# Performance work log

Hardware: AMD Instinct MI355X
Metric: run time of the kernel (lower is better)

The kernel has to match this reference:

```python
import jax, jax.numpy as jnp
import numpy as np

EPS = 1.1920929e-07  # torch clamp_probs eps for float32
TEMP = 0.3           # sampler temperature T


def conv1d(x, w, b, pad):
    # x: [B, Cin, L], w: [Cout, Cin, K] -> [B, Cout, L']
    y = jax.lax.conv_general_dilated(x, w, window_strides=(1,), padding=[(pad, pad)],
                                     dimension_numbers=('NCH', 'OIH', 'NCH'))
    return y + b[None, :, None]


def setup_inputs() -> dict:
    key = jax.random.key(0)
    ks = jax.random.split(key, 20)
    B, L, V, E, F, H, K = 512, 512, 100000, 100, 100, 100, 10
    p = lambda i, shape: jax.random.normal(ks[i], shape, jnp.float32) * 0.02
    return {
        'x': jax.random.randint(ks[0], (B, L), 0, V, dtype=jnp.int32),
        'u': jax.random.uniform(ks[1], (B, K, L), dtype=jnp.float32),
        'emb': p(2, (V, E)),
        'conv1_w': p(3, (F, E, 3)), 'conv1_b': p(4, (F,)),
        'gi_w': p(5, (H, F)), 'gi_b': p(6, (H,)),
        'conv2_w': p(7, (H, F, 3)), 'conv2_b': p(8, (H,)),
        'li_w': p(9, (H, H, 3)), 'li_b': p(10, (H,)),
        'conv3_w': p(11, (F, 2 * H, 1)), 'conv3_b': p(12, (F,)),
        'conv4_w': p(13, (1, F, 1)), 'conv4_b': p(14, (1,)),
        'fc1_w': p(15, (H, E)), 'fc1_b': p(16, (H,)),
        'head_w': p(17, (1, H)), 'head_b': p(18, (1,)),
    }


def _ti_logits(e, conv1_w, conv1_b, gi_w, gi_b, conv2_w, conv2_b,
               li_w, li_b, conv3_w, conv3_b, conv4_w, conv4_b):
    relu = jax.nn.relu
    xt = jnp.swapaxes(e, 1, 2)                       # [B, E, L]
    h = relu(conv1d(xt, conv1_w, conv1_b, 1))        # [B, F, L]
    g = relu(h.mean(axis=-1) @ gi_w.T + gi_b)        # [B, H] (AdaptiveAvgPool1d(1))
    loc = relu(conv1d(relu(conv1d(h, conv2_w, conv2_b, 1)), li_w, li_b, 1))  # [B, H, L]
    gexp = jnp.broadcast_to(g[:, :, None], loc.shape)
    z = jnp.concatenate([gexp, loc], axis=1)         # [B, 2H, L]
    z = relu(conv1d(z, conv3_w, conv3_b, 0))
    return conv1d(z, conv4_w, conv4_b, 0)            # [B, 1, L]


def reference(x, u, emb, conv1_w, conv1_b, gi_w, gi_b, conv2_w, conv2_b,
              li_w, li_b, conv3_w, conv3_b, conv4_w, conv4_b,
              fc1_w, fc1_b, head_w, head_b):
    e = emb[x]                                       # [B, L, E] embedding gather
    logits = _ti_logits(e, conv1_w, conv1_b, gi_w, gi_b, conv2_w, conv2_b,
                        li_w, li_b, conv3_w, conv3_b, conv4_w, conv4_b)
    # Gumbel top-k continuous sampling (training path)
    uc = jnp.clip(u, EPS, 1.0 - EPS)
    gumbel = -jnp.log(-jnp.log(uc))                  # [B, K, L]
    noisy = (gumbel + logits) / TEMP                 # logits [B,1,L] broadcasts over K
    csamples = jax.nn.softmax(noisy, axis=-1).max(axis=1)  # [B, L]
    # distil predictor: masked mean pooling + MLP + sigmoid head
    pooled = (e * csamples[:, :, None]).mean(axis=1)  # [B, E]
    h = jax.nn.relu(pooled @ fc1_w.T + fc1_b)
    out = jax.nn.sigmoid(h @ head_w.T + head_b)       # [B, 1]
    return out, csamples
```

## Files before the change

kernel.cpp:

```cpp
#include <hip/hip_runtime.h>
#include <math.h>

#define DEV __device__ __forceinline__

typedef __attribute__((ext_vector_type(8))) short short8;
typedef __attribute__((ext_vector_type(4))) short short4v;
typedef __attribute__((ext_vector_type(4))) float f32x4;
typedef __attribute__((ext_vector_type(2))) unsigned uint2v;

#define SSTR 136
#define ROWB (16 * SSTR * 2)

DEV short f2bf(float f) {
    unsigned u = __builtin_bit_cast(unsigned, f);
    unsigned r = (u + 0x7fffu + ((u >> 16) & 1u)) >> 16;
    return (short)r;
}

#if __has_builtin(__builtin_amdgcn_cvt_pk_bf16_f32)
DEV unsigned pk2bf(float a, float b) {
    auto v = __builtin_amdgcn_cvt_pk_bf16_f32(a, b);
    return __builtin_bit_cast(unsigned, v);
}
#else
DEV unsigned pk2bf(float a, float b) {
    return ((unsigned)(unsigned short)f2bf(a)) |
           (((unsigned)(unsigned short)f2bf(b)) << 16);
}
#endif

DEV float bfu(short s) {
    unsigned u = ((unsigned)(unsigned short)s) << 16;
    return __builtin_bit_cast(float, u);
}

__global__ __launch_bounds__(256) void prep_kernel(
    const float* __restrict__ emb, short* __restrict__ embT,
    const float* __restrict__ c1w, const float* __restrict__ c2w,
    const float* __restrict__ liw, const float* __restrict__ c3w,
    short* __restrict__ A1, short* __restrict__ A2,
    short* __restrict__ A3, short* __restrict__ A4) {
    int bxg = blockIdx.x;
    if (bxg < 12500) {
        int t = threadIdx.x;
        int row = bxg * 8 + (t >> 5);
        int c4 = t & 31;
        if (c4 >= 28) return;
        short4v v = {0, 0, 0, 0};
        if (c4 < 25) {
            f32x4 e = *(const f32x4*)&emb[row * 100 + c4 * 4];
#pragma unroll
            for (int r = 0; r < 4; ++r) v[r] = f2bf(e[r]);
        }
        *(short4v*)&embT[row * 112 + c4 * 4] = v;
        return;
    }
    if (threadIdx.x >= 64) return;
    int bx = bxg - 12500;
    const float* w; short* dst; int mode, lbx;
    if (bx < 70)       { w = c1w; dst = A1; mode = 0; lbx = bx; }
    else if (bx < 140) { w = c2w; dst = A2; mode = 0; lbx = bx - 70; }
    else if (bx < 210) { w = liw; dst = A3; mode = 0; lbx = bx - 140; }
    else               { w = c3w; dst = A4; mode = 1; lbx = bx - 210; }
    int lane = threadIdx.x;
    int f = lbx % 7 * 16 + (lane & 15);
    int kb = (lbx / 7) * 32 + (lane >> 4) * 8;
    short8 v;
#pragma unroll
    for (int j = 0; j < 8; ++j) {
        int kk = kb + j;
        float val = 0.f;
        if (f < 100) {
            if (mode == 0) {
                int oct = kk >> 3, dk = oct / 13;
                int c = (oct - 13 * dk) * 8 + (kk & 7);
                if (dk < 3 && c < 100) val = w[(f * 100 + c) * 3 + dk];
            } else {
                if (kk < 100) val = w[f * 200 + 100 + kk];
            }
        }
        v[j] = f2bf(val);
    }
    *(short8*)&dst[(lbx * 64 + lane) * 8] = v;
}

template<int MT, int NT, int MTB, int NTB, bool CLAMPL, bool POOL,
         bool TO_GLOBAL, bool EDGE>
DEV void ctap(const short* __restrict__ Ap, const short* s_src, short* s_dst,
              short* __restrict__ gout, const int* bofs, const int* bofs4,
              const float* __restrict__ bias, int row0l, int l0,
              float* __restrict__ hpart_slot, int lane) {
    const int q = lane >> 4, n = lane & 15;
    const f32x4 z4 = {0.f, 0.f, 0.f, 0.f};
    f32x4 acc[MT][NT];
#pragma unroll
    for (int mt = 0; mt < MT; ++mt) {
        int fb = (MTB + mt) * 16 + q * 4;
        f32x4 bs = (fb < 100) ? *(const f32x4*)&bias[fb] : z4;
#pragma unroll
        for (int nt = 0; nt < NT; ++nt) acc[mt][nt] = bs;
    }
#pragma unroll
    for (int ks = 0; ks < 10; ++ks) {
        short8 a[MT];
#pragma unroll
        for (int mt = 0; mt < MT; ++mt)
            a[mt] = *(const short8*)&Ap[(ks * 448 + (MTB + mt) * 64 + lane) * 8];
        const char* bp = (const char*)s_src + bofs[ks];
        short8 bf[NT];
#pragma unroll
        for (int nt = 0; nt < NT; ++nt) {
            if (CLAMPL && (NTB + nt) == 4)
                bf[nt] = *(const short8*)((const char*)s_src + bofs4[ks]);
            else
                bf[nt] = *(const short8*)(bp + (NTB + nt) * ROWB);
        }
#pragma unroll
        for (int mt = 0; mt < MT; ++mt)
#pragma unroll
            for (int nt = 0; nt < NT; ++nt)
                acc[mt][nt] = __builtin_amdgcn_mfma_f32_16x16x32_bf16(
                    a[mt], bf[nt], acc[mt][nt], 0, 0, 0);
    }
    f32x4 ps[MT];
    if constexpr (POOL) {
#pragma unroll
        for (int mt = 0; mt < MT; ++mt) ps[mt] = z4;
    }
#pragma unroll
    for (int nt = 0; nt < NT; ++nt) {
        const int j = (NTB + nt) * 16 + n;
        const int l = row0l + j;
        bool lok = true;
        if constexpr (EDGE) lok = ((unsigned)l < 512u);
        const bool pok = POOL && (l >= l0) && (l < l0 + 64);
#pragma unroll
        for (int mt = 0; mt < MT; ++mt) {
            const int fb = (MTB + mt) * 16 + q * 4;
            f32x4 v;
#pragma unroll
            for (int r = 0; r < 4; ++r) {
                v[r] = fmaxf(acc[mt][nt][r], 0.f);
                if constexpr (EDGE) v[r] = lok ? v[r] : 0.f;
            }
            if constexpr (POOL) {
                if (pok) {
#pragma unroll
                    for (int r = 0; r < 4; ++r) ps[mt][r] += v[r];
                }
            }
            uint2v pk;
            pk[0] = pk2bf(v[0], v[1]); pk[1] = pk2bf(v[2], v[3]);
            if constexpr (TO_GLOBAL) {
                *(uint2v*)&gout[j * 112 + fb] = pk;
            } else {
                if ((NTB + nt) < 4 || n < 6)
                    *(uint2v*)&s_dst[j * SSTR + fb] = pk;
            }
        }
    }
    if constexpr (POOL) {
#pragma unroll
        for (int mt = 0; mt < MT; ++mt)
#pragma unroll
            for (int off = 1; off <= 8; off <<= 1)
#pragma unroll
                for (int r = 0; r < 4; ++r)
                    ps[mt][r] += __shfl_xor(ps[mt][r], off, 64);
        if (n == 0) {
#pragma unroll
            for (int mt = 0; mt < MT; ++mt)
                *(f32x4*)&hpart_slot[(MTB + mt) * 16 + q * 4] = ps[mt];
        }
    }
}

__global__ __launch_bounds__(256, 4) void fused_conv_kernel(
    const int* __restrict__ xidx, const short* __restrict__ embT,
    const short* __restrict__ A1, const short* __restrict__ A2,
    const short* __restrict__ A3,
    const float* __restrict__ b1, const float* __restrict__ b2,
    const float* __restrict__ b3,
    short* __restrict__ locT, float* __restrict__ hpart) {
    extern __shared__ char smem[];
    short* s_e = (short*)smem;
    short* s_h = (short*)(smem + 72 * SSTR * 2);
    const int tid = threadIdx.x;
    const int b = blockIdx.y, bx = blockIdx.x, l0 = bx * 64;
    const int lane = tid & 63, wv = tid >> 6;
    const int q = lane >> 4, n = lane & 15;

#pragma unroll
    for (int p = 0; p < 5; ++p) {
        int idx = tid + p * 256;
        int j = idx >> 4, c8 = idx & 15;
        if (j < 70 && c8 < 14) {
            int lg = l0 - 3 + j;
            short8 v = {0, 0, 0, 0, 0, 0, 0, 0};
            if (lg >= 0 && lg < 512) {
                int row = xidx[b * 512 + lg];
                v = *(const short8*)&embT[row * 112 + c8 * 8];
            }
            *(short8*)&s_e[j * SSTR + c8 * 8] = v;
        }
    }

    int bofs[10], bofs4[10];
#pragma unroll
    for (int ks = 0; ks < 10; ++ks) {
        int oct = ks * 4 + q;
        int dk = (oct >= 39) ? 3 : (oct >= 26) ? 2 : (oct >= 13) ? 1 : 0;
        int c0 = (oct - 13 * dk) * 8;
        bofs[ks] = ((n + dk) * SSTR + c0) * 2;
        int r4 = 64 + n + dk; if (r4 > 69) r4 = 69;
        bofs4[ks] = (r4 * SSTR + c0) * 2;
    }
    float* hps = hpart + ((b * 8 + bx) * 2 + (wv & 1)) * 112;
    short* gouts = locT + ((size_t)b * 512 + l0) * 112;

    __syncthreads();
    const bool edge = (bx == 0) || (bx == 7);

#define PASS3T(Ap, SRC, DST, BIAS, R0L, PL, E)                                   \
    if (wv == 0)      ctap<4,3,0,0,false,PL,false,E>(Ap,SRC,DST,nullptr,bofs,bofs4,BIAS,R0L,l0,hps,lane); \
    else if (wv == 1) ctap<4,2,0,3,true, PL,false,E>(Ap,SRC,DST,nullptr,bofs,bofs4,BIAS,R0L,l0,hps,lane); \
    else if (wv == 2) ctap<3,3,4,0,false,PL,false,E>(Ap,SRC,DST,nullptr,bofs,bofs4,BIAS,R0L,l0,hps,lane); \
    else              ctap<3,2,4,3,true, PL,false,E>(Ap,SRC,DST,nullptr,bofs,bofs4,BIAS,R0L,l0,hps,lane);

    if (edge) {
        PASS3T(A1, s_e, s_h, b1, l0 - 2, true, true)
        __syncthreads();
        PASS3T(A2, s_h, s_e, b2, l0 - 1, false, true)
    } else {
        PASS3T(A1, s_e, s_h, b1, l0 - 2, true, false)
        __syncthreads();
        PASS3T(A2, s_h, s_e, b2, l0 - 1, false, false)
    }
    __syncthreads();
    if (wv == 0)      ctap<4,2,0,0,false,false,true,false>(A3,s_e,nullptr,gouts,bofs,bofs4,b3,l0,l0,hps,lane);
    else if (wv == 1) ctap<4,2,0,2,false,false,true,false>(A3,s_e,nullptr,gouts,bofs,bofs4,b3,l0,l0,hps,lane);
    else if (wv == 2) ctap<3,2,4,0,false,false,true,false>(A3,s_e,nullptr,gouts,bofs,bofs4,b3,l0,l0,hps,lane);
    else              ctap<3,2,4,2,false,false,true,false>(A3,s_e,nullptr,gouts,bofs,bofs4,b3,l0,l0,hps,lane);
#undef PASS3T
}

template<int NTB>
DEV void c3tile(const short* s_in, float* s_part, const short* __restrict__ A4,
                const float* s_zg, const float* __restrict__ w4, int lane) {
    const int q = lane >> 4, n = lane & 15;
    const f32x4 z4 = {0.f, 0.f, 0.f, 0.f};
    f32x4 acc[7][2];
#pragma unroll
    for (int mt = 0; mt < 7; ++mt) {
        int fb = mt * 16 + q * 4;
        f32x4 zgv = *(const f32x4*)&s_zg[fb];
#pragma unroll
        for (int nt = 0; nt < 2; ++nt) acc[mt][nt] = zgv;
    }
#pragma unroll
    for (int ks = 0; ks < 4; ++ks) {
        short8 a[7];
#pragma unroll
        for (int mt = 0; mt < 7; ++mt)
            a[mt] = *(const short8*)&A4[(ks * 448 + mt * 64 + lane) * 8];
        int c0 = (ks * 4 + q) * 8;
        if (c0 > 104) c0 = 104;
        const char* bp = (const char*)(s_in + n * SSTR + c0);
        short8 bf[2];
#pragma unroll
        for (int nt = 0; nt < 2; ++nt)
            bf[nt] = *(const short8*)(bp + (NTB + nt) * ROWB);
#pragma unroll
        for (int mt = 0; mt < 7; ++mt)
#pragma unroll
            for (int nt = 0; nt < 2; ++nt)
                acc[mt][nt] = __builtin_amdgcn_mfma_f32_16x16x32_bf16(
                    a[mt], bf[nt], acc[mt][nt], 0, 0, 0);
    }
#pragma unroll
    for (int nt = 0; nt < 2; ++nt) {
        float part = 0.f;
#pragma unroll
        for (int mt = 0; mt < 7; ++mt) {
            const int fb = mt * 16 + q * 4;
            f32x4 w4v = (fb < 100) ? *(const f32x4*)&w4[fb] : z4;
#pragma unroll
            for (int r = 0; r < 4; ++r)
                part += fmaxf(acc[mt][nt][r], 0.f) * w4v[r];
        }
        part += __shfl_xor(part, 16, 64);
        part += __shfl_xor(part, 32, 64);
        if (q == 0) s_part[(NTB + nt) * 16 + n] = part;
    }
}

__global__ __launch_bounds__(256, 4) void conv3_logits_kernel(
    const short* __restrict__ locT, const short* __restrict__ A4,
    const float* __restrict__ hpart, const float* __restrict__ gi_w,
    const float* __restrict__ gi_b, const float* __restrict__ w3,
    const float* __restrict__ b3, const float* __restrict__ w4,
    const float* __restrict__ b4, float* __restrict__ logits) {
    extern __shared__ char smem[];
    short* s_in = (short*)smem;
    float* s_part = (float*)(smem + 128 * SSTR * 2);
    float* s_zg = s_part + 128;
    float* s_hm = s_zg + 112;
    float* s_g = s_hm + 112;
    const int tid = threadIdx.x;
    const int b = blockIdx.y, l0r = blockIdx.x * 128;
    const int lane = tid & 63, wv = tid >> 6;

    short8 tmp[8];
#pragma unroll
    for (int p = 0; p < 8; ++p) {
        int idx = tid + p * 256;
        int j = idx >> 4, c8 = idx & 15;
        if (c8 < 14)
            tmp[p] = *(const short8*)&locT[((size_t)b * 512 + l0r + j) * 112 + c8 * 8];
    }

    if (tid < 112) {
        float a = 0.f;
#pragma unroll
        for (int s = 0; s < 16; ++s) a += hpart[(b * 16 + s) * 112 + tid];
        s_hm[tid] = a * (1.f / 512.f);
    }
    __syncthreads();
    if (tid < 100) {
        float a = gi_b[tid];
        for (int f = 0; f < 100; ++f) a += s_hm[f] * gi_w[tid * 100 + f];
        s_g[tid] = fmaxf(a, 0.f);
    }
    __syncthreads();
    if (tid < 112) {
        float a = 0.f;
        if (tid < 100) {
            a = b3[tid];
            for (int h = 0; h < 100; ++h) a += s_g[h] * w3[tid * 200 + h];
        }
        s_zg[tid] = a;
    }

#pragma unroll
    for (int p = 0; p < 8; ++p) {
        int idx = tid + p * 256;
        int j = idx >> 4, c8 = idx & 15;
        if (c8 < 14)
            *(short8*)&s_in[j * SSTR + c8 * 8] = tmp[p];
    }
    __syncthreads();
    if (wv == 0)      c3tile<0>(s_in, s_part, A4, s_zg, w4, lane);
    else if (wv == 1) c3tile<2>(s_in, s_part, A4, s_zg, w4, lane);
    else if (wv == 2) c3tile<4>(s_in, s_part, A4, s_zg, w4, lane);
    else              c3tile<6>(s_in, s_part, A4, s_zg, w4, lane);
    __syncthreads();
    if (tid < 128)
        logits[b * 512 + l0r + tid] = s_part[tid] + b4[0];
}

__global__ __launch_bounds__(256) void samp_head_kernel(
    const float* __restrict__ u, const float* __restrict__ logits,
    const int* __restrict__ xidx, const short* __restrict__ embT,
    const float* __restrict__ f1w, const float* __restrict__ f1b,
    const float* __restrict__ hw, const float* __restrict__ hb,
    float* __restrict__ cs_out, float* __restrict__ out) {
    const float EPSV = 1.1920929e-07f;
    const float INVT = 1.f / 0.3f;
    int b = blockIdx.x, tid = threadIdx.x;
    int lane = tid & 63, wv = tid >> 6;
    __shared__ float s_logT[512], s_cs[512];
    __shared__ int s_x[512];
    __shared__ float s_csw[4][512];
    __shared__ float s_acc[16][112];
    __shared__ float s_pool[112], s_h2[100], s_fin[4];
    for (int l = tid; l < 512; l += 256) {
        s_logT[l] = logits[b * 512 + l] * INVT;
        s_x[l] = xidx[b * 512 + l];
    }
    __syncthreads();
    const int nk = (wv < 2) ? 3 : 2;
    float csl[8];
#pragma unroll
    for (int i = 0; i < 8; ++i) csl[i] = 0.f;
    float lt[8];
#pragma unroll
    for (int i = 0; i < 8; ++i) lt[i] = s_logT[lane * 8 + i];
    for (int j = 0; j < nk; ++j) {
        int k = wv + 4 * j;
        f32x4 u0 = *(const f32x4*)&u[(b * 10 + k) * 512 + lane * 8];
        f32x4 u1 = *(const f32x4*)&u[(b * 10 + k) * 512 + lane * 8 + 4];
        float nz[8];
#pragma unroll
        for (int i = 0; i < 8; ++i) {
            float vv = (i < 4) ? u0[i] : u1[i - 4];
            vv = fminf(fmaxf(vv, EPSV), 1.f - EPSV);
            nz[i] = -__logf(-__logf(vv)) * INVT + lt[i];
        }
        float m = nz[0];
#pragma unroll
        for (int i = 1; i < 8; ++i) m = fmaxf(m, nz[i]);
#pragma unroll
        for (int off = 1; off <= 32; off <<= 1) m = fmaxf(m, __shfl_xor(m, off, 64));
        float e[8], s = 0.f;
#pragma unroll
        for (int i = 0; i < 8; ++i) { e[i] = __expf(nz[i] - m); s += e[i]; }
#pragma unroll
        for (int off = 1; off <= 32; off <<= 1) s += __shfl_xor(s, off, 64);
        float inv = 1.f / s;
#pragma unroll
        for (int i = 0; i < 8; ++i) csl[i] = fmaxf(csl[i], e[i] * inv);
    }
#pragma unroll
    for (int i = 0; i < 8; ++i) s_csw[wv][lane * 8 + i] = csl[i];
    __syncthreads();
    for (int l = tid; l < 512; l += 256) {
        float c = fmaxf(fmaxf(s_csw[0][l], s_csw[1][l]),
                        fmaxf(s_csw[2][l], s_csw[3][l]));
        s_cs[l] = c;
        cs_out[b * 512 + l] = c;
    }
    __syncthreads();
    int jg = tid >> 4, c8 = tid & 15;
    if (c8 < 14) {
        f32x4 pa = {0.f, 0.f, 0.f, 0.f}, pb = {0.f, 0.f, 0.f, 0.f};
#pragma unroll 4
        for (int l = jg; l < 512; l += 16) {
            int row = s_x[l];
            float cv = s_cs[l];
            short8 e8 = *(const short8*)&embT[(size_t)row * 112 + c8 * 8];
#pragma unroll
            for (int r = 0; r < 4; ++r) {
                pa[r] += cv * bfu(e8[r]);
                pb[r] += cv * bfu(e8[4 + r]);
            }
        }
        *(f32x4*)&s_acc[jg][c8 * 8] = pa;
        *(f32x4*)&s_acc[jg][c8 * 8 + 4] = pb;
    }
    __syncthreads();
    if (tid < 112) {
        float p = 0.f;
#pragma unroll
        for (int g = 0; g < 16; ++g) p += s_acc[g][tid];
        s_pool[tid] = p * (1.f / 512.f);
    }
    __syncthreads();
    if (tid < 100) {
        float a = f1b[tid];
        for (int i = 0; i < 100; ++i) a += s_pool[i] * f1w[tid * 100 + i];
        s_h2[tid] = fmaxf(a, 0.f);
    }
    __syncthreads();
    float v = (tid < 100) ? s_h2[tid] * hw[tid] : 0.f;
#pragma unroll
    for (int off = 32; off >= 1; off >>= 1) v += __shfl_xor(v, off, 64);
    if (lane == 0) s_fin[wv] = v;
    __syncthreads();
    if (tid == 0) {
        float z = s_fin[0] + s_fin[1] + s_fin[2] + s_fin[3] + hb[0];
        out[b] = 1.f / (1.f + __expf(-z));
    }
}

extern "C" void kernel_launch(void* const* d_in, const int* in_sizes, int n_in,
                              void* d_out, int out_size, void* d_ws, size_t ws_size,
                              hipStream_t stream) {
    const int*   x   = (const int*)d_in[0];
    const float* u   = (const float*)d_in[1];
    const float* emb = (const float*)d_in[2];
    const float* c1w = (const float*)d_in[3];
    const float* c1b = (const float*)d_in[4];
    const float* giw = (const float*)d_in[5];
    const float* gib = (const float*)d_in[6];
    const float* c2w = (const float*)d_in[7];
    const float* c2b = (const float*)d_in[8];
    const float* liw = (const float*)d_in[9];
    const float* lib = (const float*)d_in[10];
    const float* c3w = (const float*)d_in[11];
    const float* c3b = (const float*)d_in[12];
    const float* c4w = (const float*)d_in[13];
    const float* c4b = (const float*)d_in[14];
    const float* f1w = (const float*)d_in[15];
    const float* f1b = (const float*)d_in[16];
    const float* hww = (const float*)d_in[17];
    const float* hbb = (const float*)d_in[18];
    float* out = (float*)d_out;

    char* ws = (char*)d_ws;
    short* locT   = (short*)(ws + 0);
    short* embT   = (short*)(ws + 58720256);
    short* A1     = (short*)(ws + 81120256);
    short* A2     = (short*)(ws + 81191936);
    short* A3     = (short*)(ws + 81263616);
    short* A4     = (short*)(ws + 81335296);
    float* logits = (float*)(ws + 81593344);
    float* hpart  = (float*)(ws + 82641920);

    prep_kernel<<<12738, 256, 0, stream>>>(emb, embT, c1w, c2w, liw, c3w,
                                           A1, A2, A3, A4);

    size_t smemA = (size_t)2 * 72 * SSTR * 2;
    fused_conv_kernel<<<dim3(8, 512), 256, smemA, stream>>>(
        x, embT, A1, A2, A3, c1b, c2b, lib, locT, hpart);
    size_t smemB = (size_t)128 * SSTR * 2 + 452 * 4;
    conv3_logits_kernel<<<dim3(4, 512), 256, smemB, stream>>>(
        locT, A4, hpart, giw, gib, c3w, c3b, c4w, c4b, logits);
    samp_head_kernel<<<512, 256, 0, stream>>>(
        u, logits, x, embT, f1w, f1b, hww, hbb, out + 512, out);
}
```

Before: 263.5 us.

## Transpose small weights in prep, read conv3 input directly, widen sampler block

The prep kernel gains two blocks that pre-transpose gi_w and the global half of conv3_w, so the per-block matvecs in conv3_logits read coalesced columns. conv3_logits stops staging locT through shared memory and has the MFMA B operands load straight from global, which drops the large LDS allocation. samp_head_kernel moves to 512 threads with 8 waves, so each wave handles fewer Gumbel rows and the pooling gather has more parallelism. The trade-offs are uncoalesced per-lane global B loads in conv3 and heavier LDS use in the sampler.

```diff
diff --git a/kernel.cpp b/kernel.cpp
--- a/kernel.cpp
+++ b/kernel.cpp
@@ -38,8 +38,10 @@
     const float* __restrict__ emb, short* __restrict__ embT,
     const float* __restrict__ c1w, const float* __restrict__ c2w,
     const float* __restrict__ liw, const float* __restrict__ c3w,
+    const float* __restrict__ giw,
     short* __restrict__ A1, short* __restrict__ A2,
-    short* __restrict__ A3, short* __restrict__ A4) {
+    short* __restrict__ A3, short* __restrict__ A4,
+    float* __restrict__ giwT, float* __restrict__ w3T) {
     int bxg = blockIdx.x;
     if (bxg < 12500) {
         int t = threadIdx.x;
@@ -53,6 +55,21 @@
             for (int r = 0; r < 4; ++r) v[r] = f2bf(e[r]);
         }
         *(short4v*)&embT[row * 112 + c4 * 4] = v;
+        return;
+    }
+    if (bxg >= 12738) {
+        int t = threadIdx.x;
+        if (bxg == 12738) {
+            for (int i = t; i < 10000; i += 256) {
+                int f = i / 100, g = i % 100;
+                giwT[f * 100 + g] = giw[g * 100 + f];
+            }
+        } else {
+            for (int i = t; i < 10000; i += 256) {
+                int h = i / 100, f = i % 100;
+                w3T[h * 100 + f] = c3w[f * 200 + h];
+            }
+        }
         return;
     }
     if (threadIdx.x >= 64) return;
@@ -245,8 +262,9 @@
 }
 
 template<int NTB>
-DEV void c3tile(const short* s_in, float* s_part, const short* __restrict__ A4,
-                const float* s_zg, const float* __restrict__ w4, int lane) {
+DEV void c3tile(const short* __restrict__ locB, float* s_part,
+                const short* __restrict__ A4, const float* s_zg,
+                const float* __restrict__ w4, int lane) {
     const int q = lane >> 4, n = lane & 15;
     const f32x4 z4 = {0.f, 0.f, 0.f, 0.f};
     f32x4 acc[7][2];
@@ -265,11 +283,11 @@
             a[mt] = *(const short8*)&A4[(ks * 448 + mt * 64 + lane) * 8];
         int c0 = (ks * 4 + q) * 8;
         if (c0 > 104) c0 = 104;
-        const char* bp = (const char*)(s_in + n * SSTR + c0);
+        const short* bp = locB + n * 112 + c0;
         short8 bf[2];
 #pragma unroll
         for (int nt = 0; nt < 2; ++nt)
-            bf[nt] = *(const short8*)(bp + (NTB + nt) * ROWB);
+            bf[nt] = *(const short8*)(bp + (NTB + nt) * 16 * 112);
 #pragma unroll
         for (int mt = 0; mt < 7; ++mt)
 #pragma unroll
@@ -296,29 +314,18 @@
 
 __global__ __launch_bounds__(256, 4) void conv3_logits_kernel(
     const short* __restrict__ locT, const short* __restrict__ A4,
-    const float* __restrict__ hpart, const float* __restrict__ gi_w,
-    const float* __restrict__ gi_b, const float* __restrict__ w3,
+    const float* __restrict__ hpart, const float* __restrict__ giwT,
+    const float* __restrict__ gi_b, const float* __restrict__ w3T,
     const float* __restrict__ b3, const float* __restrict__ w4,
     const float* __restrict__ b4, float* __restrict__ logits) {
-    extern __shared__ char smem[];
-    short* s_in = (short*)smem;
-    float* s_part = (float*)(smem + 128 * SSTR * 2);
-    float* s_zg = s_part + 128;
-    float* s_hm = s_zg + 112;
-    float* s_g = s_hm + 112;
+    __shared__ float s_part[128];
+    __shared__ float s_zg[112];
+    __shared__ float s_hm[112];
+    __shared__ float s_g[100];
     const int tid = threadIdx.x;
     const int b = blockIdx.y, l0r = blockIdx.x * 128;
     const int lane = tid & 63, wv = tid >> 6;
 
-    short8 tmp[8];
-#pragma unroll
-    for (int p = 0; p < 8; ++p) {
-        int idx = tid + p * 256;
-        int j = idx >> 4, c8 = idx & 15;
-        if (c8 < 14)
-            tmp[p] = *(const short8*)&locT[((size_t)b * 512 + l0r + j) * 112 + c8 * 8];
-    }
-
     if (tid < 112) {
         float a = 0.f;
 #pragma unroll
@@ -328,7 +335,7 @@
     __syncthreads();
     if (tid < 100) {
         float a = gi_b[tid];
-        for (int f = 0; f < 100; ++f) a += s_hm[f] * gi_w[tid * 100 + f];
+        for (int f = 0; f < 100; ++f) a += s_hm[f] * giwT[f * 100 + tid];
         s_g[tid] = fmaxf(a, 0.f);
     }
     __syncthreads();
@@ -336,29 +343,23 @@
         float a = 0.f;
         if (tid < 100) {
             a = b3[tid];
-            for (int h = 0; h < 100; ++h) a += s_g[h] * w3[tid * 200 + h];
+            for (int h = 0; h < 100; ++h) a += s_g[h] * w3T[h * 100 + tid];
         }
         s_zg[tid] = a;
     }
-
-#pragma unroll
-    for (int p = 0; p < 8; ++p) {
-        int idx = tid + p * 256;
-        int j = idx >> 4, c8 = idx & 15;
-        if (c8 < 14)
-            *(short8*)&s_in[j * SSTR + c8 * 8] = tmp[p];
-    }
-    __syncthreads();
-    if (wv == 0)      c3tile<0>(s_in, s_part, A4, s_zg, w4, lane);
-    else if (wv == 1) c3tile<2>(s_in, s_part, A4, s_zg, w4, lane);
-    else if (wv == 2) c3tile<4>(s_in, s_part, A4, s_zg, w4, lane);
-    else              c3tile<6>(s_in, s_part, A4, s_zg, w4, lane);
+    __syncthreads();
+
+    const short* locB = locT + ((size_t)b * 512 + l0r) * 112;
+    if (wv == 0)      c3tile<0>(locB, s_part, A4, s_zg, w4, lane);
+    else if (wv == 1) c3tile<2>(locB, s_part, A4, s_zg, w4, lane);
+    else if (wv == 2) c3tile<4>(locB, s_part, A4, s_zg, w4, lane);
+    else              c3tile<6>(locB, s_part, A4, s_zg, w4, lane);
     __syncthreads();
     if (tid < 128)
         logits[b * 512 + l0r + tid] = s_part[tid] + b4[0];
 }
 
-__global__ __launch_bounds__(256) void samp_head_kernel(
+__global__ __launch_bounds__(512) void samp_head_kernel(
     const float* __restrict__ u, const float* __restrict__ logits,
     const int* __restrict__ xidx, const short* __restrict__ embT,
     const float* __restrict__ f1w, const float* __restrict__ f1b,
@@ -370,15 +371,15 @@
     int lane = tid & 63, wv = tid >> 6;
     __shared__ float s_logT[512], s_cs[512];
     __shared__ int s_x[512];
-    __shared__ float s_csw[4][512];
-    __shared__ float s_acc[16][112];
-    __shared__ float s_pool[112], s_h2[100], s_fin[4];
-    for (int l = tid; l < 512; l += 256) {
-        s_logT[l] = logits[b * 512 + l] * INVT;
-        s_x[l] = xidx[b * 512 + l];
-    }
-    __syncthreads();
-    const int nk = (wv < 2) ? 3 : 2;
+    __shared__ float s_csw[8][512];
+    __shared__ float s_acc[32][112];
+    __shared__ float s_pool[112], s_h2[100], s_fin[8];
+    if (tid < 512) {
+        s_logT[tid] = logits[b * 512 + tid] * INVT;
+        s_x[tid] = xidx[b * 512 + tid];
+    }
+    __syncthreads();
+    const int nk = (wv < 2) ? 2 : 1;
     float csl[8];
 #pragma unroll
     for (int i = 0; i < 8; ++i) csl[i] = 0.f;
@@ -386,7 +387,7 @@
 #pragma unroll
     for (int i = 0; i < 8; ++i) lt[i] = s_logT[lane * 8 + i];
     for (int j = 0; j < nk; ++j) {
-        int k = wv + 4 * j;
+        int k = wv + 8 * j;
         f32x4 u0 = *(const f32x4*)&u[(b * 10 + k) * 512 + lane * 8];
         f32x4 u1 = *(const f32x4*)&u[(b * 10 + k) * 512 + lane * 8 + 4];
         float nz[8];
@@ -413,18 +414,19 @@
 #pragma unroll
     for (int i = 0; i < 8; ++i) s_csw[wv][lane * 8 + i] = csl[i];
     __syncthreads();
-    for (int l = tid; l < 512; l += 256) {
-        float c = fmaxf(fmaxf(s_csw[0][l], s_csw[1][l]),
-                        fmaxf(s_csw[2][l], s_csw[3][l]));
-        s_cs[l] = c;
-        cs_out[b * 512 + l] = c;
+    if (tid < 512) {
+        float c = s_csw[0][tid];
+#pragma unroll
+        for (int w = 1; w < 8; ++w) c = fmaxf(c, s_csw[w][tid]);
+        s_cs[tid] = c;
+        cs_out[b * 512 + tid] = c;
     }
     __syncthreads();
     int jg = tid >> 4, c8 = tid & 15;
     if (c8 < 14) {
         f32x4 pa = {0.f, 0.f, 0.f, 0.f}, pb = {0.f, 0.f, 0.f, 0.f};
 #pragma unroll 4
-        for (int l = jg; l < 512; l += 16) {
+        for (int l = jg; l < 512; l += 32) {
             int row = s_x[l];
             float cv = s_cs[l];
             short8 e8 = *(const short8*)&embT[(size_t)row * 112 + c8 * 8];
@@ -441,7 +443,7 @@
     if (tid < 112) {
         float p = 0.f;
 #pragma unroll
-        for (int g = 0; g < 16; ++g) p += s_acc[g][tid];
+        for (int g = 0; g < 32; ++g) p += s_acc[g][tid];
         s_pool[tid] = p * (1.f / 512.f);
     }
     __syncthreads();
@@ -457,7 +459,9 @@
     if (lane == 0) s_fin[wv] = v;
     __syncthreads();
     if (tid == 0) {
-        float z = s_fin[0] + s_fin[1] + s_fin[2] + s_fin[3] + hb[0];
+        float z = hb[0];
+#pragma unroll
+        for (int w = 0; w < 8; ++w) z += s_fin[w];
         out[b] = 1.f / (1.f + __expf(-z));
     }
 }
@@ -495,16 +499,17 @@
     short* A4     = (short*)(ws + 81335296);
     float* logits = (float*)(ws + 81593344);
     float* hpart  = (float*)(ws + 82641920);
-
-    prep_kernel<<<12738, 256, 0, stream>>>(emb, embT, c1w, c2w, liw, c3w,
-                                           A1, A2, A3, A4);
+    float* giwT   = (float*)(ws + 86311936);
+    float* w3T    = (float*)(ws + 86351936);
+
+    prep_kernel<<<12740, 256, 0, stream>>>(emb, embT, c1w, c2w, liw, c3w, giw,
+                                           A1, A2, A3, A4, giwT, w3T);
 
     size_t smemA = (size_t)2 * 72 * SSTR * 2;
     fused_conv_kernel<<<dim3(8, 512), 256, smemA, stream>>>(
         x, embT, A1, A2, A3, c1b, c2b, lib, locT, hpart);
-    size_t smemB = (size_t)128 * SSTR * 2 + 452 * 4;
-    conv3_logits_kernel<<<dim3(4, 512), 256, smemB, stream>>>(
-        locT, A4, hpart, giw, gib, c3w, c3b, c4w, c4b, logits);
-    samp_head_kernel<<<512, 256, 0, stream>>>(
+    conv3_logits_kernel<<<dim3(4, 512), 256, 0, stream>>>(
+        locT, A4, hpart, giwT, gib, w3T, c3b, c4w, c4b, logits);
+    samp_head_kernel<<<512, 512, 0, stream>>>(
         u, logits, x, embT, f1w, f1b, hww, hbb, out + 512, out);
 }
```

Measured after the change: 263.8 us, median of 2. About the same (+0.1%).
